# Optimization experiments

Hardware: AMD Instinct MI355X
Metric: run time of the kernel (lower is better)

The kernel has to match this reference:

```python
import jax, jax.numpy as jnp
import numpy as np
import math

HID_DIM = 1024
NUM_HEADS = 8
QK_DIM = HID_DIM // 8  # 128 total, 16 per head


def setup_inputs() -> dict:
    key = jax.random.key(0)
    ks = jax.random.split(key, 7)
    B, M, C = 4, 2048, HID_DIM
    gain = math.sqrt(2.0)  # calculate_gain('relu')

    def xavier(k, fan_in, fan_out):
        std = gain * math.sqrt(2.0 / (fan_in + fan_out))
        a = math.sqrt(3.0) * std
        return jax.random.uniform(k, (fan_out, fan_in), jnp.float32, -a, a)

    x = jax.random.normal(ks[0], (B, M, C), jnp.float32)
    Wq = xavier(ks[1], C, QK_DIM)   # [out, in] like torch Linear
    Wk = xavier(ks[2], C, QK_DIM)
    Wv = xavier(ks[3], C, C)
    bq = jnp.zeros((QK_DIM,), jnp.float32)
    bk = jnp.zeros((QK_DIM,), jnp.float32)
    bv = jnp.zeros((C,), jnp.float32)
    gamma = jnp.zeros((1,), jnp.float32)
    return {"x": x, "Wq": Wq, "bq": bq, "Wk": Wk, "bk": bk,
            "Wv": Wv, "bv": bv, "gamma": gamma}


def reference(x, Wq, bq, Wk, bk, Wv, bv, gamma):
    B, M, C = x.shape
    H = NUM_HEADS
    dqk = QK_DIM // H   # per-head qk dim = 16
    dv = C // H         # per-head v dim = 128
    q = (x @ Wq.T + bq).reshape(B, M, H, dqk)  # [B,M,H,dqk]
    k = (x @ Wk.T + bk).reshape(B, M, H, dqk)
    v = (x @ Wv.T + bv).reshape(B, M, H, dv)
    scores = jnp.einsum('bmhd,bnhd->bhmn', q, k) / math.sqrt(dqk)
    scores = jnp.where(scores >= 0, scores, 0.2 * scores)  # LeakyReLU(0.2)
    beta = jax.nn.softmax(scores, axis=-1)                 # [B,H,M,M]
    out = jnp.einsum('bhmn,bnhd->bmhd', beta, v).reshape(B, M, C)
    return gamma * out + x
```

## Files before the change

### kernel.cpp

```cpp
#include <hip/hip_runtime.h>
#include <hip/hip_bf16.h>

typedef __bf16 bf16_t;
typedef __bf16 bf16x8 __attribute__((ext_vector_type(8)));
typedef float f32x4 __attribute__((ext_vector_type(4)));
typedef float f32x16 __attribute__((ext_vector_type(16)));

#define MTOT 8192
#define CDIM 1024
#define HEADS 8
#define DV 128
#define QKD 128
#define SEQ 2048
#define QSCALE 0.3606737602222409f

struct alignas(8) B4 { bf16_t a, b, c, d; };

__device__ inline bf16x8 cvt8(float4 a, float4 b) {
    bf16x8 v = { (bf16_t)a.x, (bf16_t)a.y, (bf16_t)a.z, (bf16_t)a.w,
                 (bf16_t)b.x, (bf16_t)b.y, (bf16_t)b.z, (bf16_t)b.w };
    return v;
}

__device__ inline void gl_lds16(const bf16_t* g, bf16_t* l) {
    __builtin_amdgcn_global_load_lds(
        (const __attribute__((address_space(1))) void*)g,
        (__attribute__((address_space(3))) void*)l, 16, 0, 0);
}

__device__ inline unsigned cvtpk(float a, float b) {
    unsigned r;
    asm("v_cvt_pk_bf16_f32 %0, %1, %2" : "=v"(r) : "v"(a), "v"(b));
    return r;
}

__device__ inline void plswap(unsigned& a, unsigned& b) {
    asm("v_permlane32_swap_b32 %0, %1" : "+v"(a), "+v"(b));
}

#define XITEMS (MTOT * CDIM / 8)
#define WITEMS (1280 * CDIM / 8)

__global__ __launch_bounds__(256) void cvt_all(
    const float* __restrict__ X,
    const float* __restrict__ Wq, const float* __restrict__ Wk,
    const float* __restrict__ Wv,
    bf16_t* __restrict__ Xb, bf16_t* __restrict__ Wb)
{
    int i = blockIdx.x * blockDim.x + threadIdx.x;
    if (i < XITEMS) {
        const float4* s = reinterpret_cast<const float4*>(X) + (size_t)i * 2;
        reinterpret_cast<bf16x8*>(Xb)[i] = cvt8(s[0], s[1]);
    } else {
        int j = i - XITEMS;
        const float* src;
        if (j < 16384)       src = Wq + (size_t)j * 8;
        else if (j < 32768)  src = Wk + (size_t)(j - 16384) * 8;
        else                 src = Wv + (size_t)(j - 32768) * 8;
        const float4* s = reinterpret_cast<const float4*>(src);
        reinterpret_cast<bf16x8*>(Wb)[j] = cvt8(s[0], s[1]);
    }
}

__global__ __launch_bounds__(256) void qkv_gemm3(
    const bf16_t* __restrict__ Xb, const bf16_t* __restrict__ Wb,
    const float* __restrict__ bq, const float* __restrict__ bk,
    const float* __restrict__ bv,
    bf16_t* __restrict__ Qw, bf16_t* __restrict__ Kw, bf16_t* __restrict__ Vt)
{
    __shared__ bf16_t As[128][64];
    __shared__ bf16_t Bs[128][64];

    const int tid = threadIdx.x;
    const int w = tid >> 6, l = tid & 63;
    const int c = l & 15, q = l >> 4;
    const int rw = w & 1, cw = w >> 1;
    const int bx = blockIdx.x;
    const int m0 = blockIdx.y * 128;

    const bf16_t* Arow = Xb + (size_t)(m0 + w * 8 + (l >> 3)) * CDIM + (l & 7) * 8;
    const bf16_t* Brow = Wb + (size_t)(bx * 128 + w * 8 + (l >> 3)) * CDIM + (l & 7) * 8;

    f32x4 acc[16] = {};

    for (int k0 = 0; k0 < CDIM; k0 += 64) {
        __syncthreads();
        #pragma unroll
        for (int i = 0; i < 4; ++i) {
            gl_lds16(Arow + k0 + (size_t)i * 32 * CDIM, &As[i * 32 + w * 8][0]);
            gl_lds16(Brow + k0 + (size_t)i * 32 * CDIM, &Bs[i * 32 + w * 8][0]);
        }
        __syncthreads();
        #pragma unroll
        for (int kk = 0; kk < 2; ++kk) {
            bf16x8 af[4], bfr[4];
            #pragma unroll
            for (int mt = 0; mt < 4; ++mt)
                af[mt] = *(const bf16x8*)&As[rw * 64 + mt * 16 + c][kk * 32 + q * 8];
            #pragma unroll
            for (int nt = 0; nt < 4; ++nt)
                bfr[nt] = *(const bf16x8*)&Bs[cw * 64 + nt * 16 + c][kk * 32 + q * 8];
            #pragma unroll
            for (int mt = 0; mt < 4; ++mt)
                #pragma unroll
                for (int nt = 0; nt < 4; ++nt)
                    acc[mt * 4 + nt] = __builtin_amdgcn_mfma_f32_16x16x32_bf16(
                        af[mt], bfr[nt], acc[mt * 4 + nt], 0, 0, 0);
        }
    }

    #pragma unroll
    for (int mt = 0; mt < 4; ++mt)
        #pragma unroll
        for (int nt = 0; nt < 4; ++nt) {
            const int cl = cw * 64 + nt * 16 + c;
            f32x4 a = acc[mt * 4 + nt];
            const int mg = m0 + rw * 64 + mt * 16 + q * 4;
            if (bx == 0) {
                const float bb = bq[cl];
                #pragma unroll
                for (int r = 0; r < 4; ++r)
                    Qw[(size_t)(mg + r) * QKD + cl] = (bf16_t)((a[r] + bb) * QSCALE);
            } else if (bx == 1) {
                const float bb = bk[cl];
                #pragma unroll
                for (int r = 0; r < 4; ++r)
                    Kw[(size_t)(mg + r) * QKD + cl] = (bf16_t)(a[r] + bb);
            } else {
                const int h = bx - 2;
                const float bb = bv[h * DV + cl];
                const int bidx = mg >> 11, ml = mg & 2047;
                B4 v{ (bf16_t)(a[0] + bb), (bf16_t)(a[1] + bb),
                      (bf16_t)(a[2] + bb), (bf16_t)(a[3] + bb) };
                *(B4*)(Vt + ((size_t)(bidx * HEADS + h) * DV + cl) * SEQ + ml) = v;
            }
        }
}

__global__ __launch_bounds__(256, 2) void qkv_gemm2(
    const float* __restrict__ X,
    const float* __restrict__ Wq, const float* __restrict__ bq,
    const float* __restrict__ Wk, const float* __restrict__ bk,
    const float* __restrict__ Wv, const float* __restrict__ bv,
    bf16_t* __restrict__ Qw, bf16_t* __restrict__ Kw, bf16_t* __restrict__ Vt)
{
    __shared__ alignas(16) bf16_t As[128][72];
    __shared__ alignas(16) bf16_t Bs[128][72];

    const int tid  = threadIdx.x;
    const int lane = tid & 63, wave = tid >> 6;
    const int c = lane & 15, q = lane >> 4;
    const int rw = wave & 1, cw = wave >> 1;
    const int m0 = blockIdx.y * 128;
    const int nt_idx = blockIdx.x;

    const float* W; const float* bias;
    if (nt_idx == 0)      { W = Wq; bias = bq; }
    else if (nt_idx == 1) { W = Wk; bias = bk; }
    else { W = Wv + (size_t)(nt_idx - 2) * DV * CDIM; bias = bv + (nt_idx - 2) * DV; }

    const int srow = tid >> 1, sseg = tid & 1;
    const int swr = (srow >> 3) & 3;
    const float* ax = X + (size_t)(m0 + srow) * CDIM + sseg * 32;
    const float* bxp = W + (size_t)srow * CDIM + sseg * 32;

    f32x4 acc[16] = {};

    for (int k0 = 0; k0 < CDIM; k0 += 64) {
        __syncthreads();
        #pragma unroll
        for (int i = 0; i < 4; ++i) {
            const int ph = (sseg * 4 + i) ^ swr;
            *(bf16x8*)&As[srow][ph * 8] = cvt8(*(const float4*)(ax + k0 + i * 8),
                                               *(const float4*)(ax + k0 + i * 8 + 4));
            *(bf16x8*)&Bs[srow][ph * 8] = cvt8(*(const float4*)(bxp + k0 + i * 8),
                                               *(const float4*)(bxp + k0 + i * 8 + 4));
        }
        __syncthreads();
        #pragma unroll
        for (int kk = 0; kk < 2; ++kk) {
            bf16x8 af[4], bfr[4];
            #pragma unroll
            for (int mt = 0; mt < 4; ++mt) {
                const int row = rw * 64 + mt * 16 + c;
                af[mt] = *(const bf16x8*)&As[row][((kk * 4 + q) ^ ((row >> 3) & 3)) * 8];
            }
            #pragma unroll
            for (int nt = 0; nt < 4; ++nt) {
                const int row = cw * 64 + nt * 16 + c;
                bfr[nt] = *(const bf16x8*)&Bs[row][((kk * 4 + q) ^ ((row >> 3) & 3)) * 8];
            }
            #pragma unroll
            for (int mt = 0; mt < 4; ++mt)
                #pragma unroll
                for (int nt = 0; nt < 4; ++nt)
                    acc[mt * 4 + nt] = __builtin_amdgcn_mfma_f32_16x16x32_bf16(
                        af[mt], bfr[nt], acc[mt * 4 + nt], 0, 0, 0);
        }
    }

    #pragma unroll
    for (int mt = 0; mt < 4; ++mt)
        #pragma unroll
        for (int nt = 0; nt < 4; ++nt) {
            const int col = cw * 64 + nt * 16 + c;
            const float bb = bias[col];
            f32x4 a = acc[mt * 4 + nt];
            const int mg = m0 + rw * 64 + mt * 16 + q * 4;
            if (nt_idx == 0) {
                #pragma unroll
                for (int r = 0; r < 4; ++r)
                    Qw[(size_t)(mg + r) * QKD + col] = (bf16_t)((a[r] + bb) * QSCALE);
            } else if (nt_idx == 1) {
                #pragma unroll
                for (int r = 0; r < 4; ++r)
                    Kw[(size_t)(mg + r) * QKD + col] = (bf16_t)(a[r] + bb);
            } else {
                const int h = nt_idx - 2;
                const int bidx = mg >> 11, ml = mg & 2047;
                B4 v{ (bf16_t)(a[0] + bb), (bf16_t)(a[1] + bb),
                      (bf16_t)(a[2] + bb), (bf16_t)(a[3] + bb) };
                *(B4*)(Vt + ((size_t)(bidx * HEADS + h) * DV + col) * SEQ + ml) = v;
            }
        }
}

__global__ __launch_bounds__(256, 2) void attn3(
    const bf16_t* __restrict__ Q, const bf16_t* __restrict__ K,
    const bf16_t* __restrict__ Vt, const float* __restrict__ X,
    const float* __restrict__ gptr, float* __restrict__ out)
{
    __shared__ alignas(16) bf16_t Vs[2][128][72];

    const int tid  = threadIdx.x;
    const int lane = tid & 63;
    const int c5 = lane & 31, q1 = lane >> 5;

    const int lin = blockIdx.x + (SEQ / 128) * blockIdx.y;
    const int xcd = lin & 7, jj = lin >> 3;
    const int bh = xcd * 4 + (jj >> 4);
    const int qt = jj & 15;
    const int b = bh >> 3, h = bh & 7;
    const int wave = tid >> 6;
    const int mbase = qt * 128 + wave * 32;

    const bf16x8 qf = *(const bf16x8*)(
        Q + (size_t)(b * SEQ + mbase + c5) * QKD + h * 16 + q1 * 8);

    const bf16x8 ones = { (bf16_t)1.0f, (bf16_t)1.0f, (bf16_t)1.0f, (bf16_t)1.0f,
                          (bf16_t)1.0f, (bf16_t)1.0f, (bf16_t)1.0f, (bf16_t)1.0f };

    f32x16 o[4] = {};
    f32x16 oli = {};

    const bf16_t* Vhead = Vt + (size_t)(b * HEADS + h) * DV * SEQ;
    const bf16_t* Kbase = K + (size_t)(b * SEQ) * QKD + h * 16;

    const int sdv = tid >> 1, sseg = tid & 1;
    const int swv = (sdv >> 3) & 7;

    bf16x8 vA[4], vB[4], kA[2], kB[2];

    {
        const bf16_t* s0 = Vhead + (size_t)sdv * SEQ + sseg * 32;
        #pragma unroll
        for (int i = 0; i < 4; ++i) vA[i] = *(const bf16x8*)(s0 + i * 8);
        const bf16_t* s1 = s0 + 64;
        #pragma unroll
        for (int i = 0; i < 4; ++i) vB[i] = *(const bf16x8*)(s1 + i * 8);
        #pragma unroll
        for (int blk = 0; blk < 2; ++blk) {
            kA[blk] = *(const bf16x8*)(Kbase + (size_t)(blk * 32 + c5) * QKD + q1 * 8);
            kB[blk] = *(const bf16x8*)(Kbase + (size_t)(64 + blk * 32 + c5) * QKD + q1 * 8);
        }
        #pragma unroll
        for (int i = 0; i < 4; ++i) {
            const int ph = (sseg * 4 + i) ^ swv;
            *(bf16x8*)&Vs[0][sdv][ph * 8] = vA[i];
        }
        const bf16_t* s2 = s0 + 128;
        #pragma unroll
        for (int i = 0; i < 4; ++i) vA[i] = *(const bf16x8*)(s2 + i * 8);
    }

    union U8 { bf16x8 v; unsigned u[4]; };

    #pragma unroll 1
    for (int t = 0; t < 32; t += 2) {
        #pragma unroll
        for (int half = 0; half < 2; ++half) {
            __syncthreads();
            #pragma unroll
            for (int i = 0; i < 4; ++i) {
                const int ph = (sseg * 4 + i) ^ swv;
                *(bf16x8*)&Vs[half ? 0 : 1][sdv][ph * 8] = half ? vA[i] : vB[i];
            }
            const int cur = t + half;
            const bf16x8 k0f = half ? kB[0] : kA[0];
            const bf16x8 k1f = half ? kB[1] : kA[1];
            {
                const int vt  = (cur + 3 < 32) ? cur + 3 : 31;
                const int kt2 = (cur + 2 < 32) ? cur + 2 : 31;
                const bf16_t* src = Vhead + (size_t)sdv * SEQ + vt * 64 + sseg * 32;
                #pragma unroll
                for (int i = 0; i < 4; ++i) {
                    bf16x8 vv = *(const bf16x8*)(src + i * 8);
                    if (half) vA[i] = vv; else vB[i] = vv;
                }
                #pragma unroll
                for (int blk = 0; blk < 2; ++blk) {
                    bf16x8 kk = *(const bf16x8*)(
                        Kbase + (size_t)(kt2 * 64 + blk * 32 + c5) * QKD + q1 * 8);
                    if (half) kB[blk] = kk; else kA[blk] = kk;
                }
            }

            U8 frag[4];
            #pragma unroll
            for (int blk = 0; blk < 2; ++blk) {
                f32x16 z = {};
                f32x16 s = __builtin_amdgcn_mfma_f32_32x32x16_bf16(
                    blk ? k1f : k0f, qf, z, 0, 0, 0);
                float e[16];
                #pragma unroll
                for (int r = 0; r < 16; ++r) {
                    const float sv = s[r];
                    e[r] = __builtin_amdgcn_exp2f(fmaxf(sv, 0.2f * sv));
                }
                unsigned w0 = cvtpk(e[0], e[1]),   w1 = cvtpk(e[2], e[3]);
                unsigned w2 = cvtpk(e[4], e[5]),   w3 = cvtpk(e[6], e[7]);
                unsigned w4 = cvtpk(e[8], e[9]),   w5 = cvtpk(e[10], e[11]);
                unsigned w6 = cvtpk(e[12], e[13]), w7 = cvtpk(e[14], e[15]);
                plswap(w0, w2); plswap(w1, w3);
                plswap(w4, w6); plswap(w5, w7);
                frag[blk * 2 + 0].u[0] = w0; frag[blk * 2 + 0].u[1] = w1;
                frag[blk * 2 + 0].u[2] = w2; frag[blk * 2 + 0].u[3] = w3;
                frag[blk * 2 + 1].u[0] = w4; frag[blk * 2 + 1].u[1] = w5;
                frag[blk * 2 + 1].u[2] = w6; frag[blk * 2 + 1].u[3] = w7;
            }

            __builtin_amdgcn_s_setprio(1);
            #pragma unroll
            for (int kt = 0; kt < 4; ++kt) {
                const bf16x8 pa = frag[kt].v;
                #pragma unroll
                for (int dvt = 0; dvt < 4; ++dvt) {
                    const int dv = dvt * 32 + c5;
                    const int phB = (kt * 2 + q1) ^ ((dv >> 3) & 7);
                    const bf16x8 vb = *(const bf16x8*)&Vs[half][dv][phB * 8];
                    o[dvt] = __builtin_amdgcn_mfma_f32_32x32x16_bf16(
                        pa, vb, o[dvt], 0, 0, 0);
                }
                oli = __builtin_amdgcn_mfma_f32_32x32x16_bf16(pa, ones, oli, 0, 0, 0);
            }
            __builtin_amdgcn_s_setprio(0);
        }
    }

    const float g = gptr[0];

    #pragma unroll
    for (int r = 0; r < 16; ++r) {
        const int row = (r & 3) + 8 * (r >> 2) + 4 * q1;
        const float inv = 1.f / oli[r];
        #pragma unroll
        for (int dvt = 0; dvt < 4; ++dvt) {
            const size_t idx = (size_t)(b * SEQ + mbase + row) * CDIM
                             + h * DV + dvt * 32 + c5;
            out[idx] = g * (o[dvt][r] * inv) + X[idx];
        }
    }
}

extern "C" void kernel_launch(void* const* d_in, const int* in_sizes, int n_in,
                              void* d_out, int out_size, void* d_ws, size_t ws_size,
                              hipStream_t stream) {
    const float* X  = (const float*)d_in[0];
    const float* Wq = (const float*)d_in[1];
    const float* bq = (const float*)d_in[2];
    const float* Wk = (const float*)d_in[3];
    const float* bk = (const float*)d_in[4];
    const float* Wv = (const float*)d_in[5];
    const float* bv = (const float*)d_in[6];
    const float* g  = (const float*)d_in[7];
    float* out = (float*)d_out;

    dim3 blk(256);
    const size_t big_elems = (size_t)MTOT * CDIM + 1280 * CDIM
                           + (size_t)MTOT * QKD * 2 + (size_t)MTOT * CDIM;
    const size_t big_ws = big_elems * sizeof(bf16_t);

    if (ws_size >= big_ws) {
        bf16_t* Xb = (bf16_t*)d_ws;
        bf16_t* Wb = Xb + (size_t)MTOT * CDIM;
        bf16_t* Qw = Wb + (size_t)1280 * CDIM;
        bf16_t* Kw = Qw + (size_t)MTOT * QKD;
        bf16_t* Vt = Kw + (size_t)MTOT * QKD;

        hipLaunchKernelGGL(cvt_all, dim3((XITEMS + WITEMS) / 256), blk, 0, stream,
                           X, Wq, Wk, Wv, Xb, Wb);
        hipLaunchKernelGGL(qkv_gemm3, dim3(10, 64), blk, 0, stream,
                           Xb, Wb, bq, bk, bv, Qw, Kw, Vt);
        hipLaunchKernelGGL(attn3, dim3(SEQ / 128, 32), blk, 0, stream,
                           Qw, Kw, Vt, X, g, out);
    } else {
        bf16_t* Qw = (bf16_t*)d_ws;
        bf16_t* Kw = Qw + (size_t)MTOT * QKD;
        bf16_t* Vt = Kw + (size_t)MTOT * QKD;
        hipLaunchKernelGGL(qkv_gemm2, dim3(10, 64), blk, 0, stream,
                           X, Wq, bq, Wk, bk, Wv, bv, Qw, Kw, Vt);
        hipLaunchKernelGGL(attn3, dim3(SEQ / 128, 32), blk, 0, stream,
                           Qw, Kw, Vt, X, g, out);
    }
}
```

Baseline: 206.1 us.

## Shrink QKV GEMM M-tile to 64 and compute softmax denominator with VALU sums

The QKV projection GEMM now uses 64x128 tiles with launch bounds for 4 blocks per CU. This doubles the grid to 10x128 blocks to improve occupancy and load balance, at the cost of more B-tile reloads. In the attention kernel, the row-sum MFMA against a ones vector is dropped. Each lane instead accumulates exp values in a scalar, combined with one cross-half shuffle and broadcast per row in the epilogue. This removes a fifth of the PV-stage MFMAs but adds VALU adds and shuffles.

Measured after the change: 189.6 us. 1.09x faster.

```diff
diff --git a/kernel.cpp b/kernel.cpp
--- a/kernel.cpp
+++ b/kernel.cpp
@@ -62,60 +62,60 @@
     }
 }
 
-__global__ __launch_bounds__(256) void qkv_gemm3(
+__global__ __launch_bounds__(256, 4) void qkv_gemm5(
     const bf16_t* __restrict__ Xb, const bf16_t* __restrict__ Wb,
     const float* __restrict__ bq, const float* __restrict__ bk,
     const float* __restrict__ bv,
     bf16_t* __restrict__ Qw, bf16_t* __restrict__ Kw, bf16_t* __restrict__ Vt)
 {
-    __shared__ bf16_t As[128][64];
+    __shared__ bf16_t As[64][64];
     __shared__ bf16_t Bs[128][64];
 
     const int tid = threadIdx.x;
     const int w = tid >> 6, l = tid & 63;
     const int c = l & 15, q = l >> 4;
-    const int rw = w & 1, cw = w >> 1;
     const int bx = blockIdx.x;
-    const int m0 = blockIdx.y * 128;
+    const int m0 = blockIdx.y * 64;
 
     const bf16_t* Arow = Xb + (size_t)(m0 + w * 8 + (l >> 3)) * CDIM + (l & 7) * 8;
     const bf16_t* Brow = Wb + (size_t)(bx * 128 + w * 8 + (l >> 3)) * CDIM + (l & 7) * 8;
 
-    f32x4 acc[16] = {};
+    f32x4 acc[8] = {};
 
     for (int k0 = 0; k0 < CDIM; k0 += 64) {
         __syncthreads();
         #pragma unroll
-        for (int i = 0; i < 4; ++i) {
+        for (int i = 0; i < 2; ++i)
             gl_lds16(Arow + k0 + (size_t)i * 32 * CDIM, &As[i * 32 + w * 8][0]);
+        #pragma unroll
+        for (int i = 0; i < 4; ++i)
             gl_lds16(Brow + k0 + (size_t)i * 32 * CDIM, &Bs[i * 32 + w * 8][0]);
-        }
         __syncthreads();
         #pragma unroll
         for (int kk = 0; kk < 2; ++kk) {
-            bf16x8 af[4], bfr[4];
+            bf16x8 af[4], bfr[2];
             #pragma unroll
             for (int mt = 0; mt < 4; ++mt)
-                af[mt] = *(const bf16x8*)&As[rw * 64 + mt * 16 + c][kk * 32 + q * 8];
-            #pragma unroll
-            for (int nt = 0; nt < 4; ++nt)
-                bfr[nt] = *(const bf16x8*)&Bs[cw * 64 + nt * 16 + c][kk * 32 + q * 8];
+                af[mt] = *(const bf16x8*)&As[mt * 16 + c][kk * 32 + q * 8];
+            #pragma unroll
+            for (int nt = 0; nt < 2; ++nt)
+                bfr[nt] = *(const bf16x8*)&Bs[w * 32 + nt * 16 + c][kk * 32 + q * 8];
             #pragma unroll
             for (int mt = 0; mt < 4; ++mt)
                 #pragma unroll
-                for (int nt = 0; nt < 4; ++nt)
-                    acc[mt * 4 + nt] = __builtin_amdgcn_mfma_f32_16x16x32_bf16(
-                        af[mt], bfr[nt], acc[mt * 4 + nt], 0, 0, 0);
+                for (int nt = 0; nt < 2; ++nt)
+                    acc[mt * 2 + nt] = __builtin_amdgcn_mfma_f32_16x16x32_bf16(
+                        af[mt], bfr[nt], acc[mt * 2 + nt], 0, 0, 0);
         }
     }
 
     #pragma unroll
     for (int mt = 0; mt < 4; ++mt)
         #pragma unroll
-        for (int nt = 0; nt < 4; ++nt) {
-            const int cl = cw * 64 + nt * 16 + c;
-            f32x4 a = acc[mt * 4 + nt];
-            const int mg = m0 + rw * 64 + mt * 16 + q * 4;
+        for (int nt = 0; nt < 2; ++nt) {
+            const int cl = w * 32 + nt * 16 + c;
+            f32x4 a = acc[mt * 2 + nt];
+            const int mg = m0 + mt * 16 + q * 4;
             if (bx == 0) {
                 const float bb = bq[cl];
                 #pragma unroll
@@ -247,11 +247,8 @@
     const bf16x8 qf = *(const bf16x8*)(
         Q + (size_t)(b * SEQ + mbase + c5) * QKD + h * 16 + q1 * 8);
 
-    const bf16x8 ones = { (bf16_t)1.0f, (bf16_t)1.0f, (bf16_t)1.0f, (bf16_t)1.0f,
-                          (bf16_t)1.0f, (bf16_t)1.0f, (bf16_t)1.0f, (bf16_t)1.0f };
-
+    float li = 0.f;
     f32x16 o[4] = {};
-    f32x16 oli = {};
 
     const bf16_t* Vhead = Vt + (size_t)(b * HEADS + h) * DV * SEQ;
     const bf16_t* Kbase = K + (size_t)(b * SEQ) * QKD + h * 16;
@@ -325,7 +322,9 @@
                 #pragma unroll
                 for (int r = 0; r < 16; ++r) {
                     const float sv = s[r];
-                    e[r] = __builtin_amdgcn_exp2f(fmaxf(sv, 0.2f * sv));
+                    const float ev = __builtin_amdgcn_exp2f(fmaxf(sv, 0.2f * sv));
+                    e[r] = ev;
+                    li += ev;
                 }
                 unsigned w0 = cvtpk(e[0], e[1]),   w1 = cvtpk(e[2], e[3]);
                 unsigned w2 = cvtpk(e[4], e[5]),   w3 = cvtpk(e[6], e[7]);
@@ -351,25 +350,25 @@
                     o[dvt] = __builtin_amdgcn_mfma_f32_32x32x16_bf16(
                         pa, vb, o[dvt], 0, 0, 0);
                 }
-                oli = __builtin_amdgcn_mfma_f32_32x32x16_bf16(pa, ones, oli, 0, 0, 0);
             }
             __builtin_amdgcn_s_setprio(0);
         }
     }
 
+    li += __shfl_xor(li, 32);
+    const float inv = 1.f / li;
     const float g = gptr[0];
 
     #pragma unroll
-    for (int r = 0; r < 16; ++r) {
-        const int row = (r & 3) + 8 * (r >> 2) + 4 * q1;
-        const float inv = 1.f / oli[r];
-        #pragma unroll
-        for (int dvt = 0; dvt < 4; ++dvt) {
+    for (int dvt = 0; dvt < 4; ++dvt)
+        #pragma unroll
+        for (int r = 0; r < 16; ++r) {
+            const int row = (r & 3) + 8 * (r >> 2) + 4 * q1;
+            const float linv = __shfl(inv, row);
             const size_t idx = (size_t)(b * SEQ + mbase + row) * CDIM
                              + h * DV + dvt * 32 + c5;
-            out[idx] = g * (o[dvt][r] * inv) + X[idx];
-        }
-    }
+            out[idx] = g * (o[dvt][r] * linv) + X[idx];
+        }
 }
 
 extern "C" void kernel_launch(void* const* d_in, const int* in_sizes, int n_in,
@@ -399,7 +398,7 @@
 
         hipLaunchKernelGGL(cvt_all, dim3((XITEMS + WITEMS) / 256), blk, 0, stream,
                            X, Wq, Wk, Wv, Xb, Wb);
-        hipLaunchKernelGGL(qkv_gemm3, dim3(10, 64), blk, 0, stream,
+        hipLaunchKernelGGL(qkv_gemm5, dim3(10, 128), blk, 0, stream,
                            Xb, Wb, bq, bk, bv, Qw, Kw, Vt);
         hipLaunchKernelGGL(attn3, dim3(SEQ / 128, 32), blk, 0, stream,
                            Qw, Kw, Vt, X, g, out);
```
